# Kernel tuning notes

Hardware: AMD Instinct MI355X
Metric: run time of the kernel (lower is better)

Reference implementation:

```python
import jax, jax.numpy as jnp
import numpy as np

B, C, H, W = 2, 128, 48, 48
N = H * W
NQ = 25               # number of quantization bins (r2d2 default)
K_RELIABILITY = 0.5   # self.k
A = (NQ - 1) / 2.0    # quantizer slope over score range [-1, 1]
RADIUS = 4            # label window: [x-4 : x+5, y-4 : y+5]

# ---- quantizer line coefficients (r2d2 quantized AP) ----
# first half: q1 = -a*s + (a*min + [nq..1]);  special bin 0 -> constant 1
# second half: q2 =  a*s + ([2-nq..1] - a*min); special last bin -> constant 1
_W1 = jnp.full((NQ,), -A, jnp.float32).at[0].set(0.0)
_B1 = (jnp.arange(NQ, 0, -1, dtype=jnp.float32) - A).at[0].set(1.0)
_W2 = jnp.full((NQ,), A, jnp.float32).at[-1].set(0.0)
_B2 = (jnp.arange(2 - NQ, 2, dtype=jnp.float32) + A).at[-1].set(1.0)

# ---- ground-truth label matrix (static): pixel j positive for query i iff within 9x9 window ----
_row = np.arange(N) // W
_col = np.arange(N) % W
_L = ((np.abs(_row[:, None] - _row[None, :]) <= RADIUS) &
      (np.abs(_col[:, None] - _col[None, :]) <= RADIUS)).astype(np.float32)
LABEL = jnp.asarray(_L)  # (N, N)


def grid_sample_bilinear(img, grid):
    """torch.F.grid_sample: bilinear, zero padding, align_corners=False.
    img: (C, H, W); grid: (Hg, Wg, 2) in [-1, 1] -> out (C, Hg, Wg)."""
    Ci, Hi, Wi = img.shape
    ix = ((grid[..., 0] + 1.0) * Wi - 1.0) * 0.5
    iy = ((grid[..., 1] + 1.0) * Hi - 1.0) * 0.5
    x0 = jnp.floor(ix); y0 = jnp.floor(iy)
    wx1 = ix - x0; wy1 = iy - y0

    def gather(xi, yi):
        valid = (xi >= 0) & (xi < Wi) & (yi >= 0) & (yi < Hi)
        xc = jnp.clip(xi, 0, Wi - 1).astype(jnp.int32)
        yc = jnp.clip(yi, 0, Hi - 1).astype(jnp.int32)
        return img[:, yc, xc] * valid.astype(img.dtype)  # (C, Hg, Wg)

    return (gather(x0, y0) * (1 - wx1) * (1 - wy1)
            + gather(x0 + 1, y0) * wx1 * (1 - wy1)
            + gather(x0, y0 + 1) * (1 - wx1) * wy1
            + gather(x0 + 1, y0 + 1) * wx1 * wy1)


def quantized_ap(S, labels):
    """S: (N, M) similarity scores in [-1,1]; labels: (N, M) in {0,1}. Returns AP (N,)."""
    s = S[:, None, :]                                      # (N, 1, M)
    q1 = _W1[None, :, None] * s + _B1[None, :, None]        # (N, NQ, M)
    q2 = _W2[None, :, None] * s + _B2[None, :, None]
    q = jnp.maximum(jnp.minimum(q1, q2), 0.0)               # triangular bin weights
    nbs = q.sum(-1)                                         # (N, NQ) all counts per bin
    rec = jnp.einsum('ncm,nm->nc', q, labels)               # (N, NQ) positive counts per bin
    prec = jnp.cumsum(rec, -1) / (1e-16 + jnp.cumsum(nbs, -1))
    return (prec * rec).sum(-1) / rec.sum(-1)               # (N,)


def _loss_one(query_desc, db_desc, rel_map, g):
    db = grid_sample_bilinear(db_desc, g)                   # (C, H, W)
    Q = query_desc.reshape(C, N).T                          # (N, C)
    D = db.reshape(C, N).T                                  # (M=N, C)
    S = Q @ D.T                                             # (N, M) cosine scores
    ap = quantized_ap(S, LABEL)                             # (N,)
    r = rel_map.reshape(-1)                                 # (N,)
    return jnp.mean(1.0 - (ap * r + K_RELIABILITY * (1.0 - r)))


def setup_inputs() -> dict:
    key = jax.random.key(0)
    k1, k2, k3, k4 = jax.random.split(key, 4)
    d1 = jax.random.normal(k1, (B, C, H, W), jnp.float32)
    d1 = d1 / jnp.linalg.norm(d1, axis=1, keepdims=True)
    d2 = jax.random.normal(k2, (B, C, H, W), jnp.float32)
    d2 = d2 / jnp.linalg.norm(d2, axis=1, keepdims=True)
    rel = jax.random.uniform(k3, (B, 1, H, W), jnp.float32)
    grid = jax.random.uniform(k4, (B, H, W, 2), jnp.float32, minval=-1.0, maxval=1.0)
    return {"image1_descriptor": d1, "image2_descriptor": d2,
            "reliability": rel, "grid": grid}


def reference(image1_descriptor, image2_descriptor, reliability, grid):
    per_image = jax.vmap(_loss_one)(image1_descriptor, image2_descriptor,
                                    reliability[:, 0], grid)
    return per_image.mean()
```

## Files before the change

### kernel.cpp

```cpp
#include <hip/hip_runtime.h>
#include <hip/hip_bf16.h>

#define BB 2
#define CC 128
#define HH 48
#define WW 48
#define NN (HH*WW)
#define PB 26
#define HST 27
#define QT 16
#define MT 64
#define MSPLIT 4
#define NTILES (NN/QT)
#define ITERS (NN/MSPLIT/MT)
#define SLICE (QT*PB)
#define PSCALE 65536.0f
#define PINV   (1.0f/65536.0f)

typedef __bf16 bf16x8 __attribute__((ext_vector_type(8)));
typedef float  f32x4  __attribute__((ext_vector_type(4)));
typedef unsigned short u16;
typedef unsigned int   u32;

static __device__ __forceinline__ u16 f2bf(float x) {
    __hip_bfloat16 h = __float2bfloat16(x);
    return __builtin_bit_cast(u16, h);
}

__global__ __launch_bounds__(256)
void k_prep(const float* __restrict__ img1, const float* __restrict__ img2,
            const float* __restrict__ grid, u16* __restrict__ Qt,
            u16* __restrict__ Dt, float* __restrict__ out) {
    int blk = blockIdx.x;
    if (blk == 0 && threadIdx.x == 0) out[0] = 0.0f;
    bool isg = blk >= 144;
    int bb  = isg ? blk - 144 : blk;
    int bm  = (bb >> 3) * 256 + threadIdx.x;
    int cc0 = (bb & 7) * 16;
    int b   = bm / NN;
    int p   = bm - b * NN;
    u16 tmp[16];
    if (!isg) {
        const float* im = img1 + (size_t)b * CC * NN + (size_t)cc0 * NN;
        #pragma unroll
        for (int c = 0; c < 16; ++c) tmp[c] = f2bf(im[(size_t)c * NN + p]);
        uint4* dst = reinterpret_cast<uint4*>(Qt + (size_t)bm * CC + cc0);
        dst[0] = *reinterpret_cast<uint4*>(&tmp[0]);
        dst[1] = *reinterpret_cast<uint4*>(&tmp[8]);
    } else {
        float gx = grid[bm * 2 + 0];
        float gy = grid[bm * 2 + 1];
        float ix = ((gx + 1.0f) * (float)WW - 1.0f) * 0.5f;
        float iy = ((gy + 1.0f) * (float)HH - 1.0f) * 0.5f;
        float x0f = floorf(ix), y0f = floorf(iy);
        float wx1 = ix - x0f, wy1 = iy - y0f;
        float wx0 = 1.0f - wx1, wy0 = 1.0f - wy1;
        int x0 = (int)x0f, y0 = (int)y0f;
        bool xv0 = (x0 >= 0) && (x0 < WW);
        bool xv1 = (x0 + 1 >= 0) && (x0 + 1 < WW);
        bool yv0 = (y0 >= 0) && (y0 < HH);
        bool yv1 = (y0 + 1 >= 0) && (y0 + 1 < HH);
        int x0c = min(max(x0, 0), WW - 1), x1c = min(max(x0 + 1, 0), WW - 1);
        int y0c = min(max(y0, 0), HH - 1), y1c = min(max(y0 + 1, 0), HH - 1);
        float w00 = (xv0 && yv0) ? wx0 * wy0 : 0.0f;
        float w01 = (xv1 && yv0) ? wx1 * wy0 : 0.0f;
        float w10 = (xv0 && yv1) ? wx0 * wy1 : 0.0f;
        float w11 = (xv1 && yv1) ? wx1 * wy1 : 0.0f;
        int p00 = y0c * WW + x0c, p01 = y0c * WW + x1c;
        int p10 = y1c * WW + x0c, p11 = y1c * WW + x1c;
        const float* im = img2 + (size_t)b * CC * NN + (size_t)cc0 * NN;
        #pragma unroll
        for (int c = 0; c < 16; ++c) {
            const float* pl = im + (size_t)c * NN;
            tmp[c] = f2bf(pl[p00] * w00 + pl[p01] * w01 + pl[p10] * w10 + pl[p11] * w11);
        }
        uint4* dst = reinterpret_cast<uint4*>(Dt + (size_t)bm * CC + cc0);
        dst[0] = *reinterpret_cast<uint4*>(&tmp[0]);
        dst[1] = *reinterpret_cast<uint4*>(&tmp[8]);
    }
}

__global__ __launch_bounds__(256)
void k_main(const u16* __restrict__ Qt, const u16* __restrict__ Dt,
            float* __restrict__ Hall, float* __restrict__ Hpos) {
    __shared__ u16  Qs[QT * 136];
    __shared__ u16  Ds[MT * 136];
    __shared__ float priv[256 * HST];
    __shared__ u32   poshu[QT * PB];

    int tid  = threadIdx.x;
    int bidx = blockIdx.x;
    int b     = bidx / (NTILES * MSPLIT);
    int rem   = bidx % (NTILES * MSPLIT);
    int ntile = rem / MSPLIT;
    int ms    = rem % MSPLIT;
    int n0 = ntile * QT;

    for (int i = tid; i < 256 * HST; i += 256) priv[i] = 0.0f;
    for (int i = tid; i < QT * PB; i += 256) poshu[i] = 0u;
    {
        int row = tid >> 4, col = tid & 15;
        *reinterpret_cast<uint4*>(&Qs[row * 136 + col * 8]) =
            *reinterpret_cast<const uint4*>(Qt + ((size_t)(b * NN + n0 + row)) * CC + col * 8);
    }
    int lane = tid & 63, wave = tid >> 6, quad = lane >> 4, l15 = lane & 15;
    int q  = l15;
    int n  = n0 + q;
    int rn = n / WW, cn = n % WW;
    float* ph = &priv[tid * HST];

    int mstart = ms * (NN / MSPLIT);
    for (int it = 0; it < ITERS; ++it) {
        int m0 = mstart + it * MT;
        __syncthreads();
        #pragma unroll
        for (int k = 0; k < 4; ++k) {
            int idx = tid + k * 256;
            int row = idx >> 4, col = idx & 15;
            *reinterpret_cast<uint4*>(&Ds[row * 136 + col * 8]) =
                *reinterpret_cast<const uint4*>(Dt + ((size_t)(b * NN + m0 + row)) * CC + col * 8);
        }
        __syncthreads();

        f32x4 acc = {0.f, 0.f, 0.f, 0.f};
        #pragma unroll
        for (int kc = 0; kc < 4; ++kc) {
            bf16x8 av = *reinterpret_cast<const bf16x8*>(&Ds[(wave * 16 + l15) * 136 + kc * 32 + quad * 8]);
            bf16x8 bv = *reinterpret_cast<const bf16x8*>(&Qs[l15 * 136 + kc * 32 + quad * 8]);
            acc = __builtin_amdgcn_mfma_f32_16x16x32_bf16(av, bv, acc, 0, 0, 0);
        }

        int mb = m0 + wave * 16 + quad * 4;
        #pragma unroll
        for (int i = 0; i < 4; ++i) {
            float s  = acc[i];
            float t  = fminf(fmaxf(fmaf(-12.0f, s, 12.0f), 0.0f), 24.0f);
            float cf = floorf(t);
            float f  = t - cf;
            int   c0 = (int)cf;
            float h0 = ph[c0], h1 = ph[c0 + 1];
            ph[c0]     = h0 + (1.0f - f);
            ph[c0 + 1] = h1 + f;
            int m  = mb + i;
            int rm = m / WW, cm = m - rm * WW;
            int dr = rn - rm, dc = cn - cm;
            if ((unsigned)(dr + 4) <= 8u && (unsigned)(dc + 4) <= 8u) {
                u32 w0 = (u32)(fmaf(-PSCALE, f, PSCALE) + 0.5f);
                u32 w1 = (u32)(f * PSCALE + 0.5f);
                atomicAdd(&poshu[q * PB + c0],     w0);
                atomicAdd(&poshu[q * PB + c0 + 1], w1);
            }
        }
    }
    __syncthreads();
    float* oa = Hall + (size_t)bidx * SLICE;
    float* op = Hpos + (size_t)bidx * SLICE;
    for (int idx = tid; idx < SLICE; idx += 256) {
        int c = idx >> 4, qq = idx & 15;
        float s2 = 0.0f;
        #pragma unroll
        for (int j = 0; j < 16; ++j) s2 += priv[(j * 16 + qq) * HST + c];
        oa[idx] = s2;
        op[idx] = (float)poshu[qq * PB + c] * PINV;
    }
}

__global__ __launch_bounds__(256)
void k_finalize(const float* __restrict__ Hall, const float* __restrict__ Hpos,
                const float* __restrict__ rel, float* __restrict__ out) {
    int gid = blockIdx.x * 256 + threadIdx.x;
    int b = gid / NN, nloc = gid % NN;
    int ntile = nloc >> 4, qq = nloc & 15;
    size_t base = ((size_t)(b * NTILES + ntile) * MSPLIT) * SLICE + qq;
    const float* ha = Hall + base;
    const float* hp = Hpos + base;
    float cumr = 0.f, cumn = 0.f, apn = 0.f, totr = 0.f;
    #pragma unroll
    for (int c = 0; c < 25; ++c) {
        float a = 0.f, r = 0.f;
        #pragma unroll
        for (int s = 0; s < MSPLIT; ++s) {
            a += ha[(size_t)s * SLICE + c * 16];
            r += hp[(size_t)s * SLICE + c * 16];
        }
        cumr += r; cumn += a;
        apn  += (cumr / (1e-16f + cumn)) * r;
        totr += r;
    }
    float ap = apn / totr;
    float rl = rel[gid];
    float loss = 1.0f - (ap * rl + 0.5f * (1.0f - rl));

    for (int off = 32; off > 0; off >>= 1) loss += __shfl_down(loss, off, 64);
    __shared__ float wsum[4];
    int ln = threadIdx.x & 63, wv = threadIdx.x >> 6;
    if (ln == 0) wsum[wv] = loss;
    __syncthreads();
    if (threadIdx.x == 0) {
        float t = wsum[0] + wsum[1] + wsum[2] + wsum[3];
        atomicAdd(out, t * (1.0f / (float)(BB * NN)));
    }
}

extern "C" void kernel_launch(void* const* d_in, const int* in_sizes, int n_in,
                              void* d_out, int out_size, void* d_ws, size_t ws_size,
                              hipStream_t stream) {
    const float* img1 = (const float*)d_in[0];
    const float* img2 = (const float*)d_in[1];
    const float* rel  = (const float*)d_in[2];
    const float* grid = (const float*)d_in[3];

    char* ws = (char*)d_ws;
    const size_t qt_bytes   = (size_t)BB * NN * CC * sizeof(u16);
    const size_t part_bytes = (size_t)BB * NTILES * MSPLIT * SLICE * sizeof(float);
    u16*   Qt   = (u16*)ws;
    u16*   Dt   = (u16*)(ws + qt_bytes);
    float* Hall = (float*)(ws + 2 * qt_bytes);
    float* Hpos = (float*)(ws + 2 * qt_bytes + part_bytes);

    k_prep    <<<288, 256, 0, stream>>>(img1, img2, grid, Qt, Dt, (float*)d_out);
    k_main    <<<BB * NTILES * MSPLIT, 256, 0, stream>>>(Qt, Dt, Hall, Hpos);
    k_finalize<<<(BB * NN) / 256, 256, 0, stream>>>(Hall, Hpos, rel, (float*)d_out);
}
```

Before: 98.71 us.

## Replace LDS histogram scatter with register cumulative-ramp accumulation

Accumulates the all-scores histogram in per-thread registers as a cumulative count using clamped ramps per bin, removing the per-thread LDS scatter array and its zero-init. Finalize consumes the cumulative counts directly instead of prefix-summing. This frees LDS for higher occupancy (launch bound 4) and avoids bank-conflicted read-modify-writes, at the cost of 25 ALU ops per score. It also splits grid-sample prep into more blocks and uses single-wave finalize blocks.

```diff
diff --git a/kernel.cpp b/kernel.cpp
--- a/kernel.cpp
+++ b/kernel.cpp
@@ -6,16 +6,18 @@
 #define HH 48
 #define WW 48
 #define NN (HH*WW)
+#define NB 25
 #define PB 26
-#define HST 27
 #define QT 16
 #define MT 64
 #define MSPLIT 4
 #define NTILES (NN/QT)
 #define ITERS (NN/MSPLIT/MT)
-#define SLICE (QT*PB)
+#define SLICE (QT*NB)
 #define PSCALE 65536.0f
 #define PINV   (1.0f/65536.0f)
+#define TBLK 144
+#define GBLK 288
 
 typedef __bf16 bf16x8 __attribute__((ext_vector_type(8)));
 typedef float  f32x4  __attribute__((ext_vector_type(4)));
@@ -33,21 +35,23 @@
             u16* __restrict__ Dt, float* __restrict__ out) {
     int blk = blockIdx.x;
     if (blk == 0 && threadIdx.x == 0) out[0] = 0.0f;
-    bool isg = blk >= 144;
-    int bb  = isg ? blk - 144 : blk;
-    int bm  = (bb >> 3) * 256 + threadIdx.x;
-    int cc0 = (bb & 7) * 16;
-    int b   = bm / NN;
-    int p   = bm - b * NN;
-    u16 tmp[16];
-    if (!isg) {
+    if (blk < TBLK) {
+        int bm  = (blk >> 3) * 256 + threadIdx.x;
+        int cc0 = (blk & 7) * 16;
+        int b   = bm / NN;
+        int p   = bm - b * NN;
         const float* im = img1 + (size_t)b * CC * NN + (size_t)cc0 * NN;
+        u16 tmp[16];
         #pragma unroll
         for (int c = 0; c < 16; ++c) tmp[c] = f2bf(im[(size_t)c * NN + p]);
         uint4* dst = reinterpret_cast<uint4*>(Qt + (size_t)bm * CC + cc0);
         dst[0] = *reinterpret_cast<uint4*>(&tmp[0]);
         dst[1] = *reinterpret_cast<uint4*>(&tmp[8]);
     } else {
+        int gb  = blk - TBLK;
+        int bm  = (gb >> 4) * 256 + threadIdx.x;
+        int cc0 = (gb & 15) * 8;
+        int b   = bm / NN;
         float gx = grid[bm * 2 + 0];
         float gy = grid[bm * 2 + 1];
         float ix = ((gx + 1.0f) * (float)WW - 1.0f) * 0.5f;
@@ -69,24 +73,24 @@
         int p00 = y0c * WW + x0c, p01 = y0c * WW + x1c;
         int p10 = y1c * WW + x0c, p11 = y1c * WW + x1c;
         const float* im = img2 + (size_t)b * CC * NN + (size_t)cc0 * NN;
-        #pragma unroll
-        for (int c = 0; c < 16; ++c) {
+        u16 tmp[8];
+        #pragma unroll
+        for (int c = 0; c < 8; ++c) {
             const float* pl = im + (size_t)c * NN;
             tmp[c] = f2bf(pl[p00] * w00 + pl[p01] * w01 + pl[p10] * w10 + pl[p11] * w11);
         }
-        uint4* dst = reinterpret_cast<uint4*>(Dt + (size_t)bm * CC + cc0);
-        dst[0] = *reinterpret_cast<uint4*>(&tmp[0]);
-        dst[1] = *reinterpret_cast<uint4*>(&tmp[8]);
-    }
-}
-
-__global__ __launch_bounds__(256)
+        *reinterpret_cast<uint4*>(Dt + (size_t)bm * CC + cc0) =
+            *reinterpret_cast<uint4*>(&tmp[0]);
+    }
+}
+
+__global__ __launch_bounds__(256, 4)
 void k_main(const u16* __restrict__ Qt, const u16* __restrict__ Dt,
             float* __restrict__ Hall, float* __restrict__ Hpos) {
-    __shared__ u16  Qs[QT * 136];
-    __shared__ u16  Ds[MT * 136];
-    __shared__ float priv[256 * HST];
-    __shared__ u32   poshu[QT * PB];
+    __shared__ u16 Qs[QT * 136];
+    union ShU { u16 Ds[MT * 136]; float red[4 * NB * 16]; };
+    __shared__ ShU sh;
+    __shared__ u32 poshu[QT * PB];
 
     int tid  = threadIdx.x;
     int bidx = blockIdx.x;
@@ -96,7 +100,6 @@
     int ms    = rem % MSPLIT;
     int n0 = ntile * QT;
 
-    for (int i = tid; i < 256 * HST; i += 256) priv[i] = 0.0f;
     for (int i = tid; i < QT * PB; i += 256) poshu[i] = 0u;
     {
         int row = tid >> 4, col = tid & 15;
@@ -107,7 +110,10 @@
     int q  = l15;
     int n  = n0 + q;
     int rn = n / WW, cn = n % WW;
-    float* ph = &priv[tid * HST];
+
+    float hc[NB];
+    #pragma unroll
+    for (int c = 0; c < NB; ++c) hc[c] = 0.0f;
 
     int mstart = ms * (NN / MSPLIT);
     for (int it = 0; it < ITERS; ++it) {
@@ -117,7 +123,7 @@
         for (int k = 0; k < 4; ++k) {
             int idx = tid + k * 256;
             int row = idx >> 4, col = idx & 15;
-            *reinterpret_cast<uint4*>(&Ds[row * 136 + col * 8]) =
+            *reinterpret_cast<uint4*>(&sh.Ds[row * 136 + col * 8]) =
                 *reinterpret_cast<const uint4*>(Dt + ((size_t)(b * NN + m0 + row)) * CC + col * 8);
         }
         __syncthreads();
@@ -125,26 +131,36 @@
         f32x4 acc = {0.f, 0.f, 0.f, 0.f};
         #pragma unroll
         for (int kc = 0; kc < 4; ++kc) {
-            bf16x8 av = *reinterpret_cast<const bf16x8*>(&Ds[(wave * 16 + l15) * 136 + kc * 32 + quad * 8]);
+            bf16x8 av = *reinterpret_cast<const bf16x8*>(&sh.Ds[(wave * 16 + l15) * 136 + kc * 32 + quad * 8]);
             bf16x8 bv = *reinterpret_cast<const bf16x8*>(&Qs[l15 * 136 + kc * 32 + quad * 8]);
             acc = __builtin_amdgcn_mfma_f32_16x16x32_bf16(av, bv, acc, 0, 0, 0);
         }
 
+        float x0 = fmaxf(fmaf(12.0f, acc[0], -11.0f), -23.0f);
+        float x1 = fmaxf(fmaf(12.0f, acc[1], -11.0f), -23.0f);
+        float x2 = fmaxf(fmaf(12.0f, acc[2], -11.0f), -23.0f);
+        float x3 = fmaxf(fmaf(12.0f, acc[3], -11.0f), -23.0f);
+        #pragma unroll
+        for (int c = 0; c < NB; ++c) {
+            float g01 = __builtin_amdgcn_fmed3f(x0, 0.0f, 1.0f)
+                      + __builtin_amdgcn_fmed3f(x1, 0.0f, 1.0f);
+            float g23 = __builtin_amdgcn_fmed3f(x2, 0.0f, 1.0f)
+                      + __builtin_amdgcn_fmed3f(x3, 0.0f, 1.0f);
+            hc[c] += g01 + g23;
+            x0 += 1.0f; x1 += 1.0f; x2 += 1.0f; x3 += 1.0f;
+        }
+
         int mb = m0 + wave * 16 + quad * 4;
         #pragma unroll
         for (int i = 0; i < 4; ++i) {
-            float s  = acc[i];
-            float t  = fminf(fmaxf(fmaf(-12.0f, s, 12.0f), 0.0f), 24.0f);
-            float cf = floorf(t);
-            float f  = t - cf;
-            int   c0 = (int)cf;
-            float h0 = ph[c0], h1 = ph[c0 + 1];
-            ph[c0]     = h0 + (1.0f - f);
-            ph[c0 + 1] = h1 + f;
             int m  = mb + i;
             int rm = m / WW, cm = m - rm * WW;
             int dr = rn - rm, dc = cn - cm;
             if ((unsigned)(dr + 4) <= 8u && (unsigned)(dc + 4) <= 8u) {
+                float t  = __builtin_amdgcn_fmed3f(fmaf(-12.0f, acc[i], 12.0f), 0.0f, 24.0f);
+                float cf = floorf(t);
+                float f  = t - cf;
+                int   c0 = (int)cf;
                 u32 w0 = (u32)(fmaf(-PSCALE, f, PSCALE) + 0.5f);
                 u32 w1 = (u32)(f * PSCALE + 0.5f);
                 atomicAdd(&poshu[q * PB + c0],     w0);
@@ -153,38 +169,45 @@
         }
     }
     __syncthreads();
+    #pragma unroll
+    for (int c = 0; c < NB; ++c) {
+        float v = hc[c];
+        v += __shfl_xor(v, 16, 64);
+        v += __shfl_xor(v, 32, 64);
+        if (lane < 16) sh.red[(wave * NB + c) * 16 + lane] = v;
+    }
+    __syncthreads();
     float* oa = Hall + (size_t)bidx * SLICE;
     float* op = Hpos + (size_t)bidx * SLICE;
     for (int idx = tid; idx < SLICE; idx += 256) {
         int c = idx >> 4, qq = idx & 15;
-        float s2 = 0.0f;
-        #pragma unroll
-        for (int j = 0; j < 16; ++j) s2 += priv[(j * 16 + qq) * HST + c];
+        float s2 = sh.red[c * 16 + qq]            + sh.red[(NB + c) * 16 + qq]
+                 + sh.red[(2 * NB + c) * 16 + qq] + sh.red[(3 * NB + c) * 16 + qq];
         oa[idx] = s2;
         op[idx] = (float)poshu[qq * PB + c] * PINV;
     }
 }
 
-__global__ __launch_bounds__(256)
+__global__ __launch_bounds__(64)
 void k_finalize(const float* __restrict__ Hall, const float* __restrict__ Hpos,
                 const float* __restrict__ rel, float* __restrict__ out) {
-    int gid = blockIdx.x * 256 + threadIdx.x;
+    int gid = blockIdx.x * 64 + threadIdx.x;
     int b = gid / NN, nloc = gid % NN;
     int ntile = nloc >> 4, qq = nloc & 15;
     size_t base = ((size_t)(b * NTILES + ntile) * MSPLIT) * SLICE + qq;
     const float* ha = Hall + base;
     const float* hp = Hpos + base;
-    float cumr = 0.f, cumn = 0.f, apn = 0.f, totr = 0.f;
+    float cumr = 0.f, apn = 0.f, totr = 0.f;
     #pragma unroll
-    for (int c = 0; c < 25; ++c) {
+    for (int c = 0; c < NB; ++c) {
         float a = 0.f, r = 0.f;
         #pragma unroll
         for (int s = 0; s < MSPLIT; ++s) {
             a += ha[(size_t)s * SLICE + c * 16];
             r += hp[(size_t)s * SLICE + c * 16];
         }
-        cumr += r; cumn += a;
-        apn  += (cumr / (1e-16f + cumn)) * r;
+        cumr += r;
+        apn  += (cumr / (1e-16f + a)) * r;
         totr += r;
     }
     float ap = apn / totr;
@@ -192,14 +215,7 @@
     float loss = 1.0f - (ap * rl + 0.5f * (1.0f - rl));
 
     for (int off = 32; off > 0; off >>= 1) loss += __shfl_down(loss, off, 64);
-    __shared__ float wsum[4];
-    int ln = threadIdx.x & 63, wv = threadIdx.x >> 6;
-    if (ln == 0) wsum[wv] = loss;
-    __syncthreads();
-    if (threadIdx.x == 0) {
-        float t = wsum[0] + wsum[1] + wsum[2] + wsum[3];
-        atomicAdd(out, t * (1.0f / (float)(BB * NN)));
-    }
+    if (threadIdx.x == 0) atomicAdd(out, loss * (1.0f / (float)(BB * NN)));
 }
 
 extern "C" void kernel_launch(void* const* d_in, const int* in_sizes, int n_in,
@@ -218,7 +234,7 @@
     float* Hall = (float*)(ws + 2 * qt_bytes);
     float* Hpos = (float*)(ws + 2 * qt_bytes + part_bytes);
 
-    k_prep    <<<288, 256, 0, stream>>>(img1, img2, grid, Qt, Dt, (float*)d_out);
+    k_prep    <<<TBLK + GBLK, 256, 0, stream>>>(img1, img2, grid, Qt, Dt, (float*)d_out);
     k_main    <<<BB * NTILES * MSPLIT, 256, 0, stream>>>(Qt, Dt, Hall, Hpos);
-    k_finalize<<<(BB * NN) / 256, 256, 0, stream>>>(Hall, Hpos, rel, (float*)d_out);
-}
+    k_finalize<<<(BB * NN) / 64, 64, 0, stream>>>(Hall, Hpos, rel, (float*)d_out);
+}
```

After: 136.3 us. +38.1%, slower.
